# Performance work log

Hardware: AMD Instinct MI355X
Metric: run time of the kernel (lower is better)

## Reference

```python
import jax, jax.numpy as jnp
import numpy as np

B, I, D = 256, 1152, 8   # batch, input_num_capsule, input_dim_vector
C, O = 10, 16            # num_capsule, dim_vector
NUM_ROUTING = 3
EPS = 1e-7


def squash(s, axis=-1):
    # v = ||s||^2 / (1 + ||s||^2) * s / ||s||
    n2 = jnp.sum(jnp.square(s), axis=axis, keepdims=True)
    return (n2 / (1.0 + n2)) * s / jnp.sqrt(n2 + EPS)


def setup_inputs() -> dict:
    key = jax.random.key(0)
    kx, kw = jax.random.split(key)
    x = jax.random.normal(kx, (B, I, D), dtype=jnp.float32)
    W = jax.random.normal(kw, (I, C, D, O), dtype=jnp.float32) * 0.05
    return {"x": x, "W": W}


def reference(x, W):
    # inputs_hat[b,i,c,o] = sum_d x[b,i,d] * W[i,c,d,o]
    # (the original tf.scan over batch of per-sample batch_dots == this einsum)
    inputs_hat = jnp.einsum('bid,icdo->bico', x, W)  # [B,I,C,O]

    bias = jnp.zeros((1, I, C, 1), dtype=x.dtype)    # routing logits
    outputs = None
    for r in range(NUM_ROUTING):
        c = jax.nn.softmax(bias, axis=2)             # softmax over num_capsule
        s = jnp.sum(c[..., None].squeeze(-1) * inputs_hat, axis=1, keepdims=True)  # [B,1,C,O]
        outputs = squash(s, axis=-1)                 # [B,1,C,O]
        if r != NUM_ROUTING - 1:
            bias = bias + jnp.sum(inputs_hat * outputs, axis=-1, keepdims=False)[..., None].squeeze(-1)[..., None]
    return outputs.reshape(B, C, O)
```

## Files before the change

kernel.cpp:

```cpp
#include <hip/hip_runtime.h>
#include <hip/hip_bf16.h>
#include <math.h>


#define B_ 256
#define I_ 1152
#define D_ 8
#define C_ 10
#define O_ 16
#define CO_ (C_*O_)
#define EPS_ 1e-7f

#define IC1 16
#define NIC1 (I_/IC1)
#define BT 16
#define NBT (B_/BT)
#define T1 320
#define IC3 128
#define NIC3 (I_/IC3)
#define T3 320

__global__ __launch_bounds__(T1) void k1_hat(
    const float* __restrict__ x,
    const float* __restrict__ W,
    __hip_bfloat16* __restrict__ hat,
    float* __restrict__ sPart1)
{
    __shared__ float xs[BT * IC1 * D_];
    __shared__ float sred[BT][CO_];
    const int tid = threadIdx.x;
    const int ic = blockIdx.x, bt = blockIdx.y;
    const int i0 = ic * IC1, b0 = bt * BT;

    for (int j = tid; j < BT * IC1 * D_ / 4; j += T1) {
        const int bb = j >> 5, r = j & 31;
        ((float4*)xs)[j] =
            *(const float4*)&x[(((size_t)(b0 + bb)) * I_ + i0) * D_ + r * 4];
    }
    __syncthreads();

    const int ig = tid / 80, r = tid % 80;
    const int c = r / 8, o2 = r % 8;

    float2 acc[BT];
    #pragma unroll
    for (int bb = 0; bb < BT; ++bb) acc[bb] = make_float2(0.0f, 0.0f);

    const float2* W2 = (const float2*)W;

    for (int k = 0; k < IC1 / 4; ++k) {
        const int il = ig * (IC1 / 4) + k;
        const int i = i0 + il;
        float2 wv[D_];
        const float2* wp = W2 + ((size_t)i * C_ + c) * (D_ * O_ / 2) + o2;
        #pragma unroll
        for (int d = 0; d < D_; ++d) wv[d] = wp[d * (O_ / 2)];
        #pragma unroll
        for (int bb = 0; bb < BT; ++bb) {
            const float* xp = &xs[(bb * IC1 + il) * D_];
            float h0 = 0.0f, h1 = 0.0f;
            #pragma unroll
            for (int d = 0; d < D_; ++d) {
                const float xv = xp[d];
                h0 = fmaf(xv, wv[d].x, h0);
                h1 = fmaf(xv, wv[d].y, h1);
            }
            acc[bb].x += h0; acc[bb].y += h1;
            *(__hip_bfloat162*)&hat[((size_t)(b0 + bb) * I_ + i) * CO_ + c * O_ + o2 * 2] =
                __float22bfloat162_rn(make_float2(h0, h1));
        }
    }

    if (ig == 0) {
        #pragma unroll
        for (int bb = 0; bb < BT; ++bb) {
            sred[bb][c * O_ + o2 * 2]     = acc[bb].x;
            sred[bb][c * O_ + o2 * 2 + 1] = acc[bb].y;
        }
    }
    __syncthreads();
    #pragma unroll
    for (int g = 1; g < 4; ++g) {
        if (ig == g) {
            #pragma unroll
            for (int bb = 0; bb < BT; ++bb) {
                sred[bb][c * O_ + o2 * 2]     += acc[bb].x;
                sred[bb][c * O_ + o2 * 2 + 1] += acc[bb].y;
            }
        }
        __syncthreads();
    }
    if (tid < CO_) {
        for (int bb = 0; bb < BT; ++bb)
            sPart1[((size_t)ic * B_ + (b0 + bb)) * CO_ + tid] = sred[bb][tid];
    }
}

__global__ __launch_bounds__(T3) void k_route(
    const __hip_bfloat16* __restrict__ hat,
    const float* __restrict__ veff,
    float* __restrict__ sPartR)
{
    __shared__ float pb[32][C_];
    __shared__ float sr[32][CO_ + 4];
    const int tid = threadIdx.x;
    const int il = tid / C_, c = tid % C_;
    const int ic = blockIdx.x, b = blockIdx.y;
    const int i0 = ic * IC3;

    float vr[O_];
    #pragma unroll
    for (int o = 0; o < O_; ++o) vr[o] = veff[(size_t)b * CO_ + c * O_ + o];
    float sacc[O_];
    #pragma unroll
    for (int o = 0; o < O_; ++o) sacc[o] = 0.0f;

    for (int sb = 0; sb < IC3 / 32; ++sb) {
        const int i = i0 + sb * 32 + il;
        const uint4* hp = (const uint4*)&hat[((size_t)b * I_ + i) * CO_ + c * O_];
        const uint4 ha = hp[0], hb = hp[1];
        float hf[O_];
        {
            const unsigned u[8] = {ha.x, ha.y, ha.z, ha.w, hb.x, hb.y, hb.z, hb.w};
            #pragma unroll
            for (int q = 0; q < 8; ++q) {
                hf[2 * q]     = __uint_as_float(u[q] << 16);
                hf[2 * q + 1] = __uint_as_float(u[q] & 0xffff0000u);
            }
        }
        float p = 0.0f;
        #pragma unroll
        for (int o = 0; o < O_; ++o) p = fmaf(hf[o], vr[o], p);
        pb[il][c] = p;
        __syncthreads();
        float pv[C_];
        #pragma unroll
        for (int q = 0; q < C_; ++q) pv[q] = pb[il][q];
        float m = pv[0];
        #pragma unroll
        for (int q = 1; q < C_; ++q) m = fmaxf(m, pv[q]);
        float sum = 0.0f;
        #pragma unroll
        for (int q = 0; q < C_; ++q) sum += __expf(pv[q] - m);
        const float route = __expf(p - m) * __builtin_amdgcn_rcpf(sum);
        #pragma unroll
        for (int o = 0; o < O_; ++o) sacc[o] = fmaf(route, hf[o], sacc[o]);
        __syncthreads();
    }

    #pragma unroll
    for (int o = 0; o < O_; ++o) sr[il][c * O_ + o] = sacc[o];
    __syncthreads();
    if (tid < CO_) {
        float s = 0.0f;
        #pragma unroll
        for (int k = 0; k < 32; ++k) s += sr[k][tid];
        sPartR[((size_t)ic * B_ + b) * CO_ + tid] = s;
    }
}

__global__ __launch_bounds__(640) void k_squash(
    const float* __restrict__ sPart,
    int nchunk, float scale,
    const float* __restrict__ prev,
    float* __restrict__ dst)
{
    __shared__ float red[4][CO_];
    const int b = blockIdx.x, tid = threadIdx.x;
    const int q = tid / CO_;
    const int co = tid % CO_;
    float s = 0.0f;
    for (int k = q; k < nchunk; k += 4)
        s += sPart[((size_t)k * B_ + b) * CO_ + co];
    red[q][co] = s;
    __syncthreads();
    if (tid < CO_) {
        s = (red[0][co] + red[1][co]) + (red[2][co] + red[3][co]);
        s *= scale;
        float n2 = s * s;
        n2 += __shfl_xor(n2, 1);
        n2 += __shfl_xor(n2, 2);
        n2 += __shfl_xor(n2, 4);
        n2 += __shfl_xor(n2, 8);
        const float sc = n2 / ((1.0f + n2) * sqrtf(n2 + EPS_));
        const float v = s * sc;
        dst[(size_t)b * CO_ + co] = (prev ? prev[(size_t)b * CO_ + co] : 0.0f) + v;
    }
}

#define THREADS 640
#define ILG 8
#define SUBI 4
#define CHUNK (ILG*SUBI)
#define NITER (I_/CHUNK)

__global__ __launch_bounds__(THREADS) void capsule_routing_kernel(
    const float* __restrict__ x, const float* __restrict__ W,
    float* __restrict__ out)
{
    __shared__ float bias[I_ * C_];
    __shared__ float spart[ILG][C_ * O_];
    __shared__ float sv[C_ * O_];
    __shared__ float vv[C_ * O_];
    __shared__ float ech[CHUNK][C_];
    __shared__ float scale[C_];

    const int b   = blockIdx.x;
    const int tid = threadIdx.x;
    for (int j = tid; j < I_ * C_; j += THREADS) bias[j] = 0.0f;
    const int il = tid / 80;
    const int rr = tid % 80;
    const int c  = rr / 8;
    const int o2 = rr % 8;
    const int o0 = o2 * 2;
    const float* xb = x + (size_t)b * I_ * D_;
    const float2* W2 = (const float2*)W;
    __syncthreads();
    {
        float acc0 = 0.0f, acc1 = 0.0f;
        for (int it = 0; it < NITER; ++it) {
            #pragma unroll
            for (int sub = 0; sub < SUBI; ++sub) {
                const int i = it * CHUNK + sub * ILG + il;
                const float* xi = xb + i * D_;
                const float2* wp = W2 + (i * C_ + c) * (D_ * O_ / 2) + o2;
                float h0 = 0.0f, h1 = 0.0f;
                #pragma unroll
                for (int d = 0; d < D_; ++d) {
                    float2 w = wp[d * (O_ / 2)];
                    float xv = xi[d];
                    h0 = fmaf(xv, w.x, h0);
                    h1 = fmaf(xv, w.y, h1);
                }
                acc0 += h0; acc1 += h1;
            }
        }
        spart[il][c * O_ + o0]     = acc0;
        spart[il][c * O_ + o0 + 1] = acc1;
    }
    __syncthreads();
    if (tid < C_ * O_) {
        float s = 0.0f;
        #pragma unroll
        for (int k = 0; k < ILG; ++k) s += spart[k][tid];
        sv[tid] = s * (1.0f / C_);
    }
    __syncthreads();
    if (tid < C_) {
        float n2 = 0.0f;
        #pragma unroll
        for (int o = 0; o < O_; ++o) { float t = sv[tid * O_ + o]; n2 = fmaf(t, t, n2); }
        scale[tid] = n2 / ((1.0f + n2) * sqrtf(n2 + EPS_));
    }
    __syncthreads();
    if (tid < C_ * O_) vv[tid] = sv[tid] * scale[tid / O_];
    __syncthreads();
    for (int pass = 1; pass < 3; ++pass) {
        float sa0 = 0.0f, sa1 = 0.0f;
        for (int it = 0; it < NITER; ++it) {
            float h0s[SUBI], h1s[SUBI];
            const float v0 = vv[c * O_ + o0];
            const float v1 = vv[c * O_ + o0 + 1];
            #pragma unroll
            for (int sub = 0; sub < SUBI; ++sub) {
                const int i = it * CHUNK + sub * ILG + il;
                const float* xi = xb + i * D_;
                const float2* wp = W2 + (i * C_ + c) * (D_ * O_ / 2) + o2;
                float h0 = 0.0f, h1 = 0.0f;
                #pragma unroll
                for (int d = 0; d < D_; ++d) {
                    float2 w = wp[d * (O_ / 2)];
                    float xv = xi[d];
                    h0 = fmaf(xv, w.x, h0);
                    h1 = fmaf(xv, w.y, h1);
                }
                h0s[sub] = h0; h1s[sub] = h1;
                float p = h0 * v0 + h1 * v1;
                p += __shfl_xor(p, 1);
                p += __shfl_xor(p, 2);
                p += __shfl_xor(p, 4);
                if (o2 == 0) bias[i * C_ + c] += p;
            }
            __syncthreads();
            if (tid < CHUNK * C_) {
                const int il2 = tid / C_, cc = tid % C_;
                const int i = it * CHUNK + il2;
                float m = -1e30f;
                #pragma unroll
                for (int k = 0; k < C_; ++k) m = fmaxf(m, bias[i * C_ + k]);
                ech[il2][cc] = __expf(bias[i * C_ + cc] - m);
            }
            __syncthreads();
            #pragma unroll
            for (int sub = 0; sub < SUBI; ++sub) {
                const int icx = sub * ILG + il;
                float sum = 0.0f;
                #pragma unroll
                for (int k = 0; k < C_; ++k) sum += ech[icx][k];
                const float route = ech[icx][c] / sum;
                sa0 = fmaf(route, h0s[sub], sa0);
                sa1 = fmaf(route, h1s[sub], sa1);
            }
            __syncthreads();
        }
        spart[il][c * O_ + o0]     = sa0;
        spart[il][c * O_ + o0 + 1] = sa1;
        __syncthreads();
        if (tid < C_ * O_) {
            float s = 0.0f;
            #pragma unroll
            for (int k = 0; k < ILG; ++k) s += spart[k][tid];
            sv[tid] = s;
        }
        __syncthreads();
        if (tid < C_) {
            float n2 = 0.0f;
            #pragma unroll
            for (int o = 0; o < O_; ++o) { float t = sv[tid * O_ + o]; n2 = fmaf(t, t, n2); }
            scale[tid] = n2 / ((1.0f + n2) * sqrtf(n2 + EPS_));
        }
        __syncthreads();
        if (tid < C_ * O_) vv[tid] = sv[tid] * scale[tid / O_];
        __syncthreads();
    }
    if (tid < C_ * O_) out[(size_t)b * C_ * O_ + tid] = vv[tid];
}

extern "C" void kernel_launch(void* const* d_in, const int* in_sizes, int n_in,
                              void* d_out, int out_size, void* d_ws, size_t ws_size,
                              hipStream_t stream) {
    (void)in_sizes; (void)n_in; (void)out_size;
    const float* x = (const float*)d_in[0];
    const float* W = (const float*)d_in[1];
    float* out = (float*)d_out;

    const size_t hat_b  = (size_t)B_ * I_ * CO_ * sizeof(__hip_bfloat16);
    const size_t sp1_b  = (size_t)NIC1 * B_ * CO_ * sizeof(float);
    const size_t spr_b  = (size_t)NIC3 * B_ * CO_ * sizeof(float);
    const size_t v_b    = (size_t)B_ * CO_ * sizeof(float);
    const size_t need   = hat_b + sp1_b + spr_b + 2 * v_b;

    if (ws_size >= need) {
        char* p = (char*)d_ws;
        __hip_bfloat16* hat = (__hip_bfloat16*)p;  p += hat_b;
        float* sPart1 = (float*)p;                 p += sp1_b;
        float* sPartR = (float*)p;                 p += spr_b;
        float* veff1  = (float*)p;                 p += v_b;
        float* veff2  = (float*)p;

        k1_hat<<<dim3(NIC1, NBT), T1, 0, stream>>>(x, W, hat, sPart1);
        k_squash<<<B_, 640, 0, stream>>>(sPart1, NIC1, 1.0f / C_, nullptr, veff1);
        k_route<<<dim3(NIC3, B_), T3, 0, stream>>>(hat, veff1, sPartR);
        k_squash<<<B_, 640, 0, stream>>>(sPartR, NIC3, 1.0f, veff1, veff2);
        k_route<<<dim3(NIC3, B_), T3, 0, stream>>>(hat, veff2, sPartR);
        k_squash<<<B_, 640, 0, stream>>>(sPartR, NIC3, 1.0f, nullptr, out);
    } else {
        capsule_routing_kernel<<<B_, THREADS, 0, stream>>>(x, W, out);
    }
}
```

Before: 77.13 us.

## Remap k1_hat threads to float4 output chunks with smaller batch tile

Halves the batch tile in the first kernel and remaps each thread to compute four output components with float4 weight loads and 8-byte packed bf16 stores, spreading the input capsules over 8 groups instead of 4. The goal is wider memory transactions, more blocks for occupancy, and fewer registers per thread for accumulators. In exchange, each weight load is reused over fewer batch elements, which adds weight traffic. The shared-memory reduction also grows from 4 to 8 serialized steps, each with a barrier.

Result: slower. 97.62 us (+26.6%).

```diff
diff --git a/kernel.cpp b/kernel.cpp
--- a/kernel.cpp
+++ b/kernel.cpp
@@ -13,7 +13,7 @@
 
 #define IC1 16
 #define NIC1 (I_/IC1)
-#define BT 16
+#define BT 8
 #define NBT (B_/BT)
 #define T1 320
 #define IC3 128
@@ -32,65 +32,73 @@
     const int ic = blockIdx.x, bt = blockIdx.y;
     const int i0 = ic * IC1, b0 = bt * BT;
 
-    for (int j = tid; j < BT * IC1 * D_ / 4; j += T1) {
-        const int bb = j >> 5, r = j & 31;
-        ((float4*)xs)[j] =
-            *(const float4*)&x[(((size_t)(b0 + bb)) * I_ + i0) * D_ + r * 4];
-    }
-    __syncthreads();
-
-    const int ig = tid / 80, r = tid % 80;
-    const int c = r / 8, o2 = r % 8;
-
-    float2 acc[BT];
-    #pragma unroll
-    for (int bb = 0; bb < BT; ++bb) acc[bb] = make_float2(0.0f, 0.0f);
-
-    const float2* W2 = (const float2*)W;
-
-    for (int k = 0; k < IC1 / 4; ++k) {
-        const int il = ig * (IC1 / 4) + k;
+    if (tid < BT * IC1 * D_ / 4) {
+        const int bb = tid >> 5, r = tid & 31;
+        ((float4*)xs)[tid] =
+            *(const float4*)&x[((size_t)(b0 + bb) * I_ + i0) * D_ + r * 4];
+    }
+    __syncthreads();
+
+    const int ig = tid / 40, r = tid % 40;
+    const int c = r / 4, o4 = r % 4;
+
+    float4 acc[BT];
+    #pragma unroll
+    for (int bb = 0; bb < BT; ++bb) acc[bb] = make_float4(0.f, 0.f, 0.f, 0.f);
+
+    const float4* W4 = (const float4*)W;
+
+    #pragma unroll
+    for (int k = 0; k < 2; ++k) {
+        const int il = ig * 2 + k;
         const int i = i0 + il;
-        float2 wv[D_];
-        const float2* wp = W2 + ((size_t)i * C_ + c) * (D_ * O_ / 2) + o2;
-        #pragma unroll
-        for (int d = 0; d < D_; ++d) wv[d] = wp[d * (O_ / 2)];
+        float4 wv[D_];
+        const float4* wp = W4 + ((size_t)i * C_ + c) * (D_ * O_ / 4) + o4;
+        #pragma unroll
+        for (int d = 0; d < D_; ++d) wv[d] = wp[d * (O_ / 4)];
         #pragma unroll
         for (int bb = 0; bb < BT; ++bb) {
             const float* xp = &xs[(bb * IC1 + il) * D_];
-            float h0 = 0.0f, h1 = 0.0f;
+            float4 h = make_float4(0.f, 0.f, 0.f, 0.f);
             #pragma unroll
             for (int d = 0; d < D_; ++d) {
                 const float xv = xp[d];
-                h0 = fmaf(xv, wv[d].x, h0);
-                h1 = fmaf(xv, wv[d].y, h1);
-            }
-            acc[bb].x += h0; acc[bb].y += h1;
-            *(__hip_bfloat162*)&hat[((size_t)(b0 + bb) * I_ + i) * CO_ + c * O_ + o2 * 2] =
-                __float22bfloat162_rn(make_float2(h0, h1));
+                h.x = fmaf(xv, wv[d].x, h.x);
+                h.y = fmaf(xv, wv[d].y, h.y);
+                h.z = fmaf(xv, wv[d].z, h.z);
+                h.w = fmaf(xv, wv[d].w, h.w);
+            }
+            acc[bb].x += h.x; acc[bb].y += h.y;
+            acc[bb].z += h.z; acc[bb].w += h.w;
+            union { __hip_bfloat162 h2[2]; uint2 u; } pk;
+            pk.h2[0] = __float22bfloat162_rn(make_float2(h.x, h.y));
+            pk.h2[1] = __float22bfloat162_rn(make_float2(h.z, h.w));
+            *(uint2*)&hat[((size_t)(b0 + bb) * I_ + i) * CO_ + c * O_ + o4 * 4] = pk.u;
         }
     }
 
     if (ig == 0) {
         #pragma unroll
-        for (int bb = 0; bb < BT; ++bb) {
-            sred[bb][c * O_ + o2 * 2]     = acc[bb].x;
-            sred[bb][c * O_ + o2 * 2 + 1] = acc[bb].y;
-        }
-    }
-    __syncthreads();
-    #pragma unroll
-    for (int g = 1; g < 4; ++g) {
+        for (int bb = 0; bb < BT; ++bb)
+            *(float4*)&sred[bb][c * O_ + o4 * 4] = acc[bb];
+    }
+    __syncthreads();
+    #pragma unroll
+    for (int g = 1; g < 8; ++g) {
         if (ig == g) {
             #pragma unroll
             for (int bb = 0; bb < BT; ++bb) {
-                sred[bb][c * O_ + o2 * 2]     += acc[bb].x;
-                sred[bb][c * O_ + o2 * 2 + 1] += acc[bb].y;
+                float4* sp = (float4*)&sred[bb][c * O_ + o4 * 4];
+                float4 t = *sp;
+                t.x += acc[bb].x; t.y += acc[bb].y;
+                t.z += acc[bb].z; t.w += acc[bb].w;
+                *sp = t;
             }
         }
         __syncthreads();
     }
     if (tid < CO_) {
+        #pragma unroll
         for (int bb = 0; bb < BT; ++bb)
             sPart1[((size_t)ic * B_ + (b0 + bb)) * CO_ + tid] = sred[bb][tid];
     }
```
